# Optimization experiments

Measured on AMD Instinct MI355X. Metric: run time of the kernel, lower is better.

Reference implementation:

```python
import jax, jax.numpy as jnp
import numpy as np

NUM_HEADS = 16

def setup_inputs() -> dict:
    key = jax.random.key(0)
    ks = jax.random.split(key, 5)
    B, T, C = 2, 2048, 1024
    s = 0.02
    return {
        "x": jax.random.normal(ks[0], (B, T, C), dtype=jnp.float32),
        "in_w": jax.random.normal(ks[1], (3 * C, C), dtype=jnp.float32) * s,
        "in_b": jax.random.normal(ks[2], (3 * C,), dtype=jnp.float32) * s,
        "out_w": jax.random.normal(ks[3], (C, C), dtype=jnp.float32) * s,
        "out_b": jax.random.normal(ks[4], (C,), dtype=jnp.float32) * s,
    }

def reference(x, in_w, in_b, out_w, out_b):
    B, T, C = x.shape
    H = NUM_HEADS
    D = C // H
    qvk = x @ in_w.T + in_b  # (B, T, 3C)
    # einops 'b t (d k h) -> k b h t d': factor 3C as (D, 3, H), D outermost
    qvk = qvk.reshape(B, T, D, 3, H).transpose(3, 0, 4, 1, 2)  # (3, B, H, T, D)
    q, v, k = qvk[0], qvk[1], qvk[2]  # note q, v, k assignment order
    scores = jnp.einsum('bhid,bhjd->bhij', q, k) * (D ** -0.5)  # (B, H, T, T)
    causal = jnp.tril(jnp.ones((T, T), dtype=bool))
    scores = jnp.where(causal, scores, -jnp.inf)
    attn = jax.nn.softmax(scores, axis=-1)
    out = jnp.einsum('bhij,bhjd->bhid', attn, v)  # (B, H, T, D)
    out = out.transpose(0, 2, 1, 3).reshape(B, T, C)  # 'b h t d -> b t (h d)'
    return out @ out_w.T + out_b
```

## Files before the change

kernel.cpp:

```cpp
#include <hip/hip_runtime.h>


#define BB 2
#define TT 2048
#define CC 1024
#define HH 16
#define DD 64
#define MM (BB*TT)
#define N3 (3*CC)
#define BH (BB*HH)
#define KSCALE 0.18033688011112042f

typedef unsigned short u16;
typedef unsigned int   u32;
typedef __bf16 bf16x8 __attribute__((ext_vector_type(8)));
typedef float  f32x4  __attribute__((ext_vector_type(4)));

__device__ __forceinline__ u16 f32_to_bf16(float f) {
  u32 u = __float_as_uint(f);
  return (u16)((u + 0x7fffu + ((u >> 16) & 1u)) >> 16);
}
__device__ __forceinline__ u32 pack2_bf16(float a, float b) {
  u32 ua = __float_as_uint(a) + 0x8000u;
  u32 ub = __float_as_uint(b) + 0x8000u;
  return __builtin_amdgcn_perm(ub, ua, 0x07060302);
}

#define N4_X  (MM * CC / 4)
#define N4_W  (N3 * CC / 4)
#define N4_OW (CC * CC / 4)
__global__ __launch_bounds__(256) void cast_all(const float* __restrict__ x,
                                                const float* __restrict__ in_w,
                                                const float* __restrict__ out_w,
                                                u16* __restrict__ xb,
                                                u16* __restrict__ wb,
                                                u16* __restrict__ owb) {
  int i = blockIdx.x * 256 + threadIdx.x;
  const float* src; u16* dst; int j; int sj;
  if (i < N4_X)             { src = x;     dst = xb;  j = i;               sj = j; }
  else if (i < N4_X + N4_W) { src = in_w;  dst = wb;  j = i - N4_X;
                              int rp = j >> 8, c = j & 255;
                              int s = rp >> 10, h = (rp >> 6) & 15, d = rp & 63;
                              sj = (d * 48 + s * 16 + h) * 256 + c; }
  else                      { src = out_w; dst = owb; j = i - N4_X - N4_W; sj = j; }
  float4 f = reinterpret_cast<const float4*>(src)[sj];
  uint2 pk;
  pk.x = (u32)f32_to_bf16(f.x) | ((u32)f32_to_bf16(f.y) << 16);
  pk.y = (u32)f32_to_bf16(f.z) | ((u32)f32_to_bf16(f.w) << 16);
  reinterpret_cast<uint2*>(dst)[j] = pk;
}

__device__ __forceinline__ void gemm_core(const u16* __restrict__ Ag,
                                          const u16* __restrict__ Bg,
                                          int K, u16* Al, u16* Bl,
                                          int m0, int n0, f32x4 acc[4][4]) {
  const int tid = threadIdx.x, lane = tid & 63, w = tid >> 6;
  const int quad = lane >> 4, colr = lane & 15;
  const int mw = (w >> 1) * 64, nw = (w & 1) * 64;
  const int srow = lane >> 3, scol = lane & 7;
  const uint4* Al4 = reinterpret_cast<const uint4*>(Al);
  const uint4* Bl4 = reinterpret_cast<const uint4*>(Bl);
  for (int kt = 0; kt < K / 64; ++kt) {
    __syncthreads();
    #pragma unroll
    for (int ii = 0; ii < 4; ++ii) {
      int inst = w * 4 + ii;
      int row = inst * 8 + srow;
      int cs = scol ^ (row & 7);
      const u16* ga = Ag + (size_t)(m0 + row) * K + kt * 64 + cs * 8;
      const u16* gb = Bg + (size_t)(n0 + row) * K + kt * 64 + cs * 8;
      __builtin_amdgcn_global_load_lds(
          (const __attribute__((address_space(1))) void*)ga,
          (__attribute__((address_space(3))) void*)(Al + inst * 512), 16, 0, 0);
      __builtin_amdgcn_global_load_lds(
          (const __attribute__((address_space(1))) void*)gb,
          (__attribute__((address_space(3))) void*)(Bl + inst * 512), 16, 0, 0);
    }
    __syncthreads();
    #pragma unroll
    for (int ks = 0; ks < 2; ++ks) {
      bf16x8 af[4], bfr[4];
      #pragma unroll
      for (int t = 0; t < 4; ++t) {
        int mrow = mw + t * 16 + colr;
        af[t]  = __builtin_bit_cast(bf16x8, Al4[mrow * 8 + ((ks * 4 + quad) ^ (mrow & 7))]);
        int nrow = nw + t * 16 + colr;
        bfr[t] = __builtin_bit_cast(bf16x8, Bl4[nrow * 8 + ((ks * 4 + quad) ^ (nrow & 7))]);
      }
      #pragma unroll
      for (int mt = 0; mt < 4; ++mt)
        #pragma unroll
        for (int nt = 0; nt < 4; ++nt)
          acc[mt][nt] = __builtin_amdgcn_mfma_f32_16x16x32_bf16(af[mt], bfr[nt], acc[mt][nt], 0, 0, 0);
    }
  }
}

__global__ __launch_bounds__(256) void gemm_qkv(const u16* __restrict__ xb,
                                                const u16* __restrict__ wb,
                                                const float* __restrict__ in_b,
                                                u16* __restrict__ qkv) {
  __shared__ __align__(16) u16 Al[128 * 64];
  __shared__ __align__(16) u16 Bl[128 * 64];
  const int lane = threadIdx.x & 63, w = threadIdx.x >> 6;
  const int quad = lane >> 4, colr = lane & 15;
  const int mw = (w >> 1) * 64, nw = (w & 1) * 64;
  const int m0 = blockIdx.x * 128, n0 = blockIdx.y * 128;
  f32x4 acc[4][4];
  #pragma unroll
  for (int mt = 0; mt < 4; ++mt)
    #pragma unroll
    for (int nt = 0; nt < 4; ++nt) acc[mt][nt] = (f32x4){0.f, 0.f, 0.f, 0.f};
  gemm_core(xb, wb, CC, Al, Bl, m0, n0, acc);
  const int b_ = m0 >> 11;
  #pragma unroll
  for (int nt = 0; nt < 4; ++nt) {
    int np = n0 + nw + nt * 16 + colr;
    int s = np >> 10, h = (np >> 6) & 15, d = np & 63;
    float bias = in_b[d * 48 + s * 16 + h];
    float sc = (s == 2) ? KSCALE : 1.0f;
    u16* base = qkv + ((size_t)(s * BH + b_ * HH + h) * TT) * DD + d;
    #pragma unroll
    for (int mt = 0; mt < 4; ++mt)
      #pragma unroll
      for (int e = 0; e < 4; ++e) {
        int t = (m0 + mw + mt * 16 + quad * 4 + e) & (TT - 1);
        base[(size_t)t * DD] = f32_to_bf16((acc[mt][nt][e] + bias) * sc);
      }
  }
}

__global__ __launch_bounds__(128, 4) void attn_mfma(const u16* __restrict__ qkv,
                                                    float* __restrict__ po,
                                                    float* __restrict__ pl) {
  __shared__ __align__(16) u32 Vt[64 * 36];
  __shared__ __align__(16) u32 Pl[2 * 32 * 36];
  const int tid  = threadIdx.x;
  const int lane = tid & 63, w = tid >> 6;
  const int quad = lane >> 4, colr = lane & 15;
  const int f = blockIdx.x;
  const int qq = (f >> 3) & 3;
  const int pr = (f >> 5) & 15;
  const int bh = (f & 7) * 4 + (f >> 9);

  const uint4* Qg4 = reinterpret_cast<const uint4*>(qkv + (size_t)bh * TT * DD);
  const uint4* Vg4 = reinterpret_cast<const uint4*>(qkv + ((size_t)BH + bh) * TT * DD);
  const uint4* Kg4 = reinterpret_cast<const uint4*>(qkv + ((size_t)2 * BH + bh) * TT * DD);
  const uint4* Vt4 = reinterpret_cast<const uint4*>(Vt);
  const uint4* Pl4 = reinterpret_cast<const uint4*>(Pl);

  const int s_jp = tid & 31, s_half = tid >> 5;
  const int wb32 = w * (32 * 36);

  const int vlo = (qq == 0) ? 0 : (qq * 8 + 1);
  const int vhi = qq * 8 + 8;
  int sqt[2], sjlo[2], sjhi[2], nseg = 0;
  if (vlo <= pr) { sqt[nseg] = pr; sjlo[nseg] = vlo; sjhi[nseg] = vhi < pr ? vhi : pr; ++nseg; }
  if (vhi > pr)  { sqt[nseg] = 31 - pr;
                   int lo = (vlo > pr + 1 ? vlo : pr + 1) - (pr + 1);
                   sjlo[nseg] = lo; sjhi[nseg] = vhi - (pr + 1); ++nseg; }

  for (int sg = 0; sg < nseg; ++sg) {
    const int qt = sqt[sg], jlo = sjlo[sg], jhi = sjhi[sg];
    const int i0 = qt * 64;

    bf16x8 qa[2][2];
    #pragma unroll
    for (int u = 0; u < 2; ++u)
      #pragma unroll
      for (int ks = 0; ks < 2; ++ks)
        qa[u][ks] = __builtin_bit_cast(bf16x8,
            Qg4[(size_t)(i0 + w * 32 + u * 16 + colr) * 8 + ks * 4 + quad]);

    f32x4 oacc[2][4];
    #pragma unroll
    for (int u = 0; u < 2; ++u)
      #pragma unroll
      for (int dt = 0; dt < 4; ++dt) oacc[u][dt] = (f32x4){0.f, 0.f, 0.f, 0.f};
    float lp[2] = {0.f, 0.f};

    uint4 va[2], vb[2];
    #pragma unroll
    for (int io = 0; io < 2; ++io) {
      va[io] = Vg4[(size_t)(jlo * 64 + 2 * s_jp) * 8 + s_half + io * 4];
      vb[io] = Vg4[(size_t)(jlo * 64 + 2 * s_jp + 1) * 8 + s_half + io * 4];
    }

    for (int jt = jlo; jt <= jhi; ++jt) {
      const int j0 = jt * 64;
      __syncthreads();
      #pragma unroll
      for (int io = 0; io < 2; ++io) {
        const int oc = s_half + io * 4;
        u32 aw[4] = {va[io].x, va[io].y, va[io].z, va[io].w};
        u32 bw[4] = {vb[io].x, vb[io].y, vb[io].z, vb[io].w};
        #pragma unroll
        for (int m = 0; m < 4; ++m) {
          Vt[(oc * 8 + 2 * m)     * 36 + s_jp] = __builtin_amdgcn_perm(bw[m], aw[m], 0x05040100);
          Vt[(oc * 8 + 2 * m + 1) * 36 + s_jp] = __builtin_amdgcn_perm(bw[m], aw[m], 0x07060302);
        }
      }
      if (jt < jhi) {
        int nj = j0 + 64;
        #pragma unroll
        for (int io = 0; io < 2; ++io) {
          va[io] = Vg4[(size_t)(nj + 2 * s_jp) * 8 + s_half + io * 4];
          vb[io] = Vg4[(size_t)(nj + 2 * s_jp + 1) * 8 + s_half + io * 4];
        }
      }
      __syncthreads();

      f32x4 sacc[2][4];
      #pragma unroll
      for (int u = 0; u < 2; ++u)
        #pragma unroll
        for (int t4 = 0; t4 < 4; ++t4) sacc[u][t4] = (f32x4){0.f, 0.f, 0.f, 0.f};
      #pragma unroll
      for (int ks = 0; ks < 2; ++ks) {
        uint4 kk[4];
        #pragma unroll
        for (int t4 = 0; t4 < 4; ++t4)
          kk[t4] = Kg4[(size_t)(j0 + t4 * 16 + colr) * 8 + ks * 4 + quad];
        #pragma unroll
        for (int t4 = 0; t4 < 4; ++t4) {
          bf16x8 kb = __builtin_bit_cast(bf16x8, kk[t4]);
          #pragma unroll
          for (int u = 0; u < 2; ++u)
            sacc[u][t4] = __builtin_amdgcn_mfma_f32_16x16x32_bf16(kb, qa[u][ks], sacc[u][t4], 0, 0, 0);
        }
      }

      if (jt == qt) {
        #pragma unroll
        for (int u = 0; u < 2; ++u) {
          const int qv = w * 32 + u * 16 + colr;
          #pragma unroll
          for (int t4 = 0; t4 < 4; ++t4) {
            float p0 = __builtin_amdgcn_exp2f(sacc[u][t4][0]);
            float p1 = __builtin_amdgcn_exp2f(sacc[u][t4][1]);
            float p2 = __builtin_amdgcn_exp2f(sacc[u][t4][2]);
            float p3 = __builtin_amdgcn_exp2f(sacc[u][t4][3]);
            int jb = t4 * 16 + quad * 4;
            if (jb + 0 > qv) p0 = 0.f;
            if (jb + 1 > qv) p1 = 0.f;
            if (jb + 2 > qv) p2 = 0.f;
            if (jb + 3 > qv) p3 = 0.f;
            lp[u] += (p0 + p1) + (p2 + p3);
            uint2 pw; pw.x = pack2_bf16(p0, p1); pw.y = pack2_bf16(p2, p3);
            *reinterpret_cast<uint2*>(Pl + wb32 + (u * 16 + colr) * 36 + t4 * 8 + quad * 2) = pw;
          }
        }
      } else {
        #pragma unroll
        for (int u = 0; u < 2; ++u)
          #pragma unroll
          for (int t4 = 0; t4 < 4; ++t4) {
            float p0 = __builtin_amdgcn_exp2f(sacc[u][t4][0]);
            float p1 = __builtin_amdgcn_exp2f(sacc[u][t4][1]);
            float p2 = __builtin_amdgcn_exp2f(sacc[u][t4][2]);
            float p3 = __builtin_amdgcn_exp2f(sacc[u][t4][3]);
            lp[u] += (p0 + p1) + (p2 + p3);
            uint2 pw; pw.x = pack2_bf16(p0, p1); pw.y = pack2_bf16(p2, p3);
            *reinterpret_cast<uint2*>(Pl + wb32 + (u * 16 + colr) * 36 + t4 * 8 + quad * 2) = pw;
          }
      }

      #pragma unroll
      for (int u = 0; u < 2; ++u) {
        bf16x8 pa[2];
        #pragma unroll
        for (int ks = 0; ks < 2; ++ks)
          pa[ks] = __builtin_bit_cast(bf16x8,
              Pl4[(wb32 + (u * 16 + colr) * 36 + ks * 16 + quad * 4) >> 2]);
        #pragma unroll
        for (int dt = 0; dt < 4; ++dt)
          #pragma unroll
          for (int ks = 0; ks < 2; ++ks) {
            bf16x8 vfr = __builtin_bit_cast(bf16x8, Vt4[(dt * 16 + colr) * 9 + ks * 4 + quad]);
            oacc[u][dt] = __builtin_amdgcn_mfma_f32_16x16x32_bf16(pa[ks], vfr, oacc[u][dt], 0, 0, 0);
          }
      }
    }

    const int slot = bh * 32 + qt;
    float* ob = po + (size_t)slot * 4096;
    #pragma unroll
    for (int u = 0; u < 2; ++u) {
      float ls = lp[u];
      ls += __shfl_xor(ls, 16);
      ls += __shfl_xor(ls, 32);
      if (quad == 0) atomicAdd(&pl[slot * 64 + w * 32 + u * 16 + colr], ls);
      #pragma unroll
      for (int dt = 0; dt < 4; ++dt)
        #pragma unroll
        for (int rg = 0; rg < 4; ++rg)
          atomicAdd(&ob[(w * 32 + u * 16 + quad * 4 + rg) * 64 + dt * 16 + colr],
                    oacc[u][dt][rg]);
    }
  }
}

__global__ __launch_bounds__(256) void attn_finalize(const float* __restrict__ po,
                                                     const float* __restrict__ pl,
                                                     u16* __restrict__ ab) {
  const int slot = blockIdx.x;
  const int bh = slot >> 5, qt = slot & 31;
  const int b_ = bh >> 4, h = bh & 15;
  const int t = threadIdx.x;
  const int r = t >> 2, dq = t & 3;
  const float4* o4 = reinterpret_cast<const float4*>(po + (size_t)slot * 4096 + r * 64 + dq * 16);
  float inv = 1.0f / pl[slot * 64 + r];
  u16* dst = ab + ((size_t)(b_ * TT + qt * 64 + r)) * CC + h * DD + dq * 16;
  #pragma unroll
  for (int c = 0; c < 4; ++c) {
    float4 a = o4[c];
    uint2 pk;
    pk.x = pack2_bf16(a.x * inv, a.y * inv);
    pk.y = pack2_bf16(a.z * inv, a.w * inv);
    *reinterpret_cast<uint2*>(dst + c * 4) = pk;
  }
}

__global__ __launch_bounds__(256) void gemm_out(const u16* __restrict__ ab,
                                                const u16* __restrict__ owb,
                                                const float* __restrict__ out_b,
                                                float* __restrict__ out) {
  __shared__ __align__(16) u16 Al[128 * 64];
  __shared__ __align__(16) u16 Bl[128 * 64];
  const int lane = threadIdx.x & 63, w = threadIdx.x >> 6;
  const int quad = lane >> 4, colr = lane & 15;
  const int mw = (w >> 1) * 64, nw = (w & 1) * 64;
  const int m0 = blockIdx.x * 128, n0 = blockIdx.y * 128;
  f32x4 acc[4][4];
  #pragma unroll
  for (int mt = 0; mt < 4; ++mt)
    #pragma unroll
    for (int nt = 0; nt < 4; ++nt) acc[mt][nt] = (f32x4){0.f, 0.f, 0.f, 0.f};
  gemm_core(ab, owb, CC, Al, Bl, m0, n0, acc);
  float bias[4];
  #pragma unroll
  for (int nt = 0; nt < 4; ++nt) bias[nt] = out_b[n0 + nw + nt * 16 + colr];
  #pragma unroll
  for (int mt = 0; mt < 4; ++mt)
    #pragma unroll
    for (int e = 0; e < 4; ++e) {
      int row = m0 + mw + mt * 16 + quad * 4 + e;
      #pragma unroll
      for (int nt = 0; nt < 4; ++nt)
        out[(size_t)row * CC + n0 + nw + nt * 16 + colr] = acc[mt][nt][e] + bias[nt];
    }
}

extern "C" void kernel_launch(void* const* d_in, const int* in_sizes, int n_in,
                              void* d_out, int out_size, void* d_ws, size_t ws_size,
                              hipStream_t stream) {
  const float* x     = (const float*)d_in[0];
  const float* in_w  = (const float*)d_in[1];
  const float* in_b  = (const float*)d_in[2];
  const float* out_w = (const float*)d_in[3];
  const float* out_b = (const float*)d_in[4];
  float* out = (float*)d_out;

  char* ws = (char*)d_ws;
  u16* xb   = (u16*)(ws + 0);
  u16* ab   = (u16*)(ws + 0);
  u16* wb   = (u16*)(ws + 8388608);
  u16* owb  = (u16*)(ws + 14680064);
  float* po = (float*)(ws + 16777216);
  float* pl = (float*)(ws + 16777216 + 16777216);
  u16* qkv  = (u16*)(ws + 41943040);

  hipMemsetAsync(po, 0, 16777216 + 262144, stream);
  cast_all<<<dim3((N4_X + N4_W + N4_OW) / 256), 256, 0, stream>>>(x, in_w, out_w, xb, wb, owb);

  gemm_qkv<<<dim3(MM / 128, N3 / 128), 256, 0, stream>>>(xb, wb, in_b, qkv);
  attn_mfma<<<dim3(2048), 128, 0, stream>>>(qkv, po, pl);
  attn_finalize<<<dim3(1024), 256, 0, stream>>>(po, pl, ab);
  gemm_out<<<dim3(MM / 128, CC / 128), 256, 0, stream>>>(ab, owb, out_b, out);
}
```

Baseline: 246.4 us.

## Rebalance causal attention split to drop atomics and memset, double-buffer V tile

Each attention block now covers a pair of query tiles (pr and 31-pr) split into two halves. Query tiles whose whole key range is handled by one block write normalized bf16 output directly. The other half writes plain partial sums to unique slots, which a smaller finalize pass adds and normalizes. This removes the float atomics, the workspace memset and half of the finalize work. The V transpose buffer is double-buffered to drop one barrier per key tile. The cost is more LDS per block, a lower occupancy hint and half as many blocks.

```diff
diff --git a/kernel.cpp b/kernel.cpp
--- a/kernel.cpp
+++ b/kernel.cpp
@@ -130,38 +130,36 @@
   }
 }
 
-__global__ __launch_bounds__(128, 4) void attn_mfma(const u16* __restrict__ qkv,
+__global__ __launch_bounds__(128, 2) void attn_mfma(const u16* __restrict__ qkv,
+                                                    u16* __restrict__ aout,
                                                     float* __restrict__ po,
                                                     float* __restrict__ pl) {
-  __shared__ __align__(16) u32 Vt[64 * 36];
+  __shared__ __align__(16) u32 Vt[2][64 * 36];
   __shared__ __align__(16) u32 Pl[2 * 32 * 36];
   const int tid  = threadIdx.x;
   const int lane = tid & 63, w = tid >> 6;
   const int quad = lane >> 4, colr = lane & 15;
   const int f = blockIdx.x;
-  const int qq = (f >> 3) & 3;
-  const int pr = (f >> 5) & 15;
-  const int bh = (f & 7) * 4 + (f >> 9);
+  const int hf = (f >> 3) & 1;
+  const int pr = (f >> 4) & 15;
+  const int bh = (f & 7) * 4 + (f >> 8);
+  const int b_ = bh >> 4, h = bh & 15;
+  const int slot = (((bh << 4) + pr) << 1) | hf;
 
   const uint4* Qg4 = reinterpret_cast<const uint4*>(qkv + (size_t)bh * TT * DD);
   const uint4* Vg4 = reinterpret_cast<const uint4*>(qkv + ((size_t)BH + bh) * TT * DD);
   const uint4* Kg4 = reinterpret_cast<const uint4*>(qkv + ((size_t)2 * BH + bh) * TT * DD);
-  const uint4* Vt4 = reinterpret_cast<const uint4*>(Vt);
   const uint4* Pl4 = reinterpret_cast<const uint4*>(Pl);
 
   const int s_jp = tid & 31, s_half = tid >> 5;
   const int wb32 = w * (32 * 36);
 
-  const int vlo = (qq == 0) ? 0 : (qq * 8 + 1);
-  const int vhi = qq * 8 + 8;
-  int sqt[2], sjlo[2], sjhi[2], nseg = 0;
-  if (vlo <= pr) { sqt[nseg] = pr; sjlo[nseg] = vlo; sjhi[nseg] = vhi < pr ? vhi : pr; ++nseg; }
-  if (vhi > pr)  { sqt[nseg] = 31 - pr;
-                   int lo = (vlo > pr + 1 ? vlo : pr + 1) - (pr + 1);
-                   sjlo[nseg] = lo; sjhi[nseg] = vhi - (pr + 1); ++nseg; }
-
+  const int nseg = 2 - hf;
   for (int sg = 0; sg < nseg; ++sg) {
-    const int qt = sqt[sg], jlo = sjlo[sg], jhi = sjhi[sg];
+    const bool final_out = (hf == 0) && (sg == 0);
+    const int qt  = final_out ? pr : (31 - pr);
+    const int jlo = (hf == 1) ? (16 - pr) : 0;
+    const int jhi = (hf == 1) ? (31 - pr) : (sg == 0 ? pr : 15 - pr);
     const int i0 = qt * 64;
 
     bf16x8 qa[2][2];
@@ -188,7 +186,9 @@
 
     for (int jt = jlo; jt <= jhi; ++jt) {
       const int j0 = jt * 64;
-      __syncthreads();
+      u32* vtw = Vt[jt & 1];
+      const uint4* vt4 = reinterpret_cast<const uint4*>(Vt[jt & 1]);
+
       #pragma unroll
       for (int io = 0; io < 2; ++io) {
         const int oc = s_half + io * 4;
@@ -196,8 +196,8 @@
         u32 bw[4] = {vb[io].x, vb[io].y, vb[io].z, vb[io].w};
         #pragma unroll
         for (int m = 0; m < 4; ++m) {
-          Vt[(oc * 8 + 2 * m)     * 36 + s_jp] = __builtin_amdgcn_perm(bw[m], aw[m], 0x05040100);
-          Vt[(oc * 8 + 2 * m + 1) * 36 + s_jp] = __builtin_amdgcn_perm(bw[m], aw[m], 0x07060302);
+          vtw[(oc * 8 + 2 * m)     * 36 + s_jp] = __builtin_amdgcn_perm(bw[m], aw[m], 0x05040100);
+          vtw[(oc * 8 + 2 * m + 1) * 36 + s_jp] = __builtin_amdgcn_perm(bw[m], aw[m], 0x07060302);
         }
       }
       if (jt < jhi) {
@@ -276,47 +276,64 @@
         for (int dt = 0; dt < 4; ++dt)
           #pragma unroll
           for (int ks = 0; ks < 2; ++ks) {
-            bf16x8 vfr = __builtin_bit_cast(bf16x8, Vt4[(dt * 16 + colr) * 9 + ks * 4 + quad]);
+            bf16x8 vfr = __builtin_bit_cast(bf16x8, vt4[(dt * 16 + colr) * 9 + ks * 4 + quad]);
             oacc[u][dt] = __builtin_amdgcn_mfma_f32_16x16x32_bf16(pa[ks], vfr, oacc[u][dt], 0, 0, 0);
           }
       }
     }
 
-    const int slot = bh * 32 + qt;
-    float* ob = po + (size_t)slot * 4096;
     #pragma unroll
     for (int u = 0; u < 2; ++u) {
       float ls = lp[u];
       ls += __shfl_xor(ls, 16);
       ls += __shfl_xor(ls, 32);
-      if (quad == 0) atomicAdd(&pl[slot * 64 + w * 32 + u * 16 + colr], ls);
-      #pragma unroll
-      for (int dt = 0; dt < 4; ++dt)
+      if (final_out) {
+        float linv[4];
         #pragma unroll
         for (int rg = 0; rg < 4; ++rg)
-          atomicAdd(&ob[(w * 32 + u * 16 + quad * 4 + rg) * 64 + dt * 16 + colr],
-                    oacc[u][dt][rg]);
-    }
+          linv[rg] = 1.0f / __shfl(ls, quad * 4 + rg);
+        #pragma unroll
+        for (int dt = 0; dt < 4; ++dt)
+          #pragma unroll
+          for (int rg = 0; rg < 4; ++rg) {
+            int ig = i0 + w * 32 + u * 16 + quad * 4 + rg;
+            size_t off = ((size_t)(b_ * TT + ig)) * CC + h * DD + dt * 16 + colr;
+            aout[off] = (u16)((__float_as_uint(oacc[u][dt][rg] * linv[rg]) + 0x8000u) >> 16);
+          }
+      } else {
+        float* ob = po + (size_t)slot * 4096;
+        #pragma unroll
+        for (int dt = 0; dt < 4; ++dt)
+          #pragma unroll
+          for (int rg = 0; rg < 4; ++rg)
+            ob[(w * 32 + u * 16 + quad * 4 + rg) * 64 + dt * 16 + colr] = oacc[u][dt][rg];
+        if (quad == 0) pl[slot * 64 + w * 32 + u * 16 + colr] = ls;
+      }
+    }
+    __syncthreads();
   }
 }
 
 __global__ __launch_bounds__(256) void attn_finalize(const float* __restrict__ po,
                                                      const float* __restrict__ pl,
                                                      u16* __restrict__ ab) {
-  const int slot = blockIdx.x;
-  const int bh = slot >> 5, qt = slot & 31;
+  const int blk = blockIdx.x;
+  const int bh = blk >> 4, pr = blk & 15;
+  const int qt = 31 - pr;
   const int b_ = bh >> 4, h = bh & 15;
   const int t = threadIdx.x;
   const int r = t >> 2, dq = t & 3;
-  const float4* o4 = reinterpret_cast<const float4*>(po + (size_t)slot * 4096 + r * 64 + dq * 16);
-  float inv = 1.0f / pl[slot * 64 + r];
+  const size_t s0 = (size_t)blk * 2, s1 = s0 + 1;
+  const float4* o0 = reinterpret_cast<const float4*>(po + s0 * 4096 + r * 64 + dq * 16);
+  const float4* o1 = reinterpret_cast<const float4*>(po + s1 * 4096 + r * 64 + dq * 16);
+  float inv = 1.0f / (pl[s0 * 64 + r] + pl[s1 * 64 + r]);
   u16* dst = ab + ((size_t)(b_ * TT + qt * 64 + r)) * CC + h * DD + dq * 16;
   #pragma unroll
   for (int c = 0; c < 4; ++c) {
-    float4 a = o4[c];
+    float4 a = o0[c], b = o1[c];
     uint2 pk;
-    pk.x = pack2_bf16(a.x * inv, a.y * inv);
-    pk.y = pack2_bf16(a.z * inv, a.w * inv);
+    pk.x = pack2_bf16((a.x + b.x) * inv, (a.y + b.y) * inv);
+    pk.y = pack2_bf16((a.z + b.z) * inv, (a.w + b.w) * inv);
     *reinterpret_cast<uint2*>(dst + c * 4) = pk;
   }
 }
@@ -370,11 +387,10 @@
   float* pl = (float*)(ws + 16777216 + 16777216);
   u16* qkv  = (u16*)(ws + 41943040);
 
-  hipMemsetAsync(po, 0, 16777216 + 262144, stream);
   cast_all<<<dim3((N4_X + N4_W + N4_OW) / 256), 256, 0, stream>>>(x, in_w, out_w, xb, wb, owb);
 
   gemm_qkv<<<dim3(MM / 128, N3 / 128), 256, 0, stream>>>(xb, wb, in_b, qkv);
-  attn_mfma<<<dim3(2048), 128, 0, stream>>>(qkv, po, pl);
-  attn_finalize<<<dim3(1024), 256, 0, stream>>>(po, pl, ab);
+  attn_mfma<<<dim3(1024), 128, 0, stream>>>(qkv, ab, po, pl);
+  attn_finalize<<<dim3(512), 256, 0, stream>>>(po, pl, ab);
   gemm_out<<<dim3(MM / 128, CC / 128), 256, 0, stream>>>(ab, owb, out_b, out);
 }
```

New measurement: 205.0 us. 1.2x faster.
